# Performance work log

Measured on AMD Instinct MI355X. Metric: run time of the kernel, lower is better.

Reference implementation:

```python
import jax, jax.numpy as jnp
import numpy as np

B = 4096       # batch
D = 256        # num_features
H = 512        # proposal_hidden_units
K = 10         # mixture_components
C = 64         # context_units
L = 4          # proposal_residual_blocks
S = 10         # num_importance_samples (call default)
HEAD = 3 * K + C
LOG2PI = float(np.log(2.0 * np.pi))


def setup_inputs() -> dict:
    key = jax.random.key(0)
    ks = jax.random.split(key, 10)
    x = jax.random.normal(ks[0], (B, D), jnp.float32)
    observed_mask = (jax.random.uniform(ks[1], (B, D)) < 0.5).astype(jnp.float32)
    s_in = 1.0 / np.sqrt(2 * D)
    s_h = 1.0 / np.sqrt(H)
    W_in = (jax.random.normal(ks[2], (2 * D, H), jnp.float32) * s_in)
    b_in = jnp.zeros((H,), jnp.float32)
    W1 = jax.random.normal(ks[3], (L, H, H), jnp.float32) * s_h
    b1 = jnp.zeros((L, H), jnp.float32)
    W2 = jax.random.normal(ks[4], (L, H, H), jnp.float32) * s_h
    b2 = jnp.zeros((L, H), jnp.float32)
    W_fin = jax.random.normal(ks[5], (H, D * HEAD), jnp.float32) * s_h
    b_fin = jnp.zeros((D * HEAD,), jnp.float32)
    return {
        "x": x, "observed_mask": observed_mask,
        "W_in": W_in, "b_in": b_in,
        "W1": W1, "b1": b1, "W2": W2, "b2": b2,
        "W_fin": W_fin, "b_fin": b_fin,
        "num_importance_samples": S,
    }


def _proposal_params(x_o, observed_mask, W_in, b_in, W1, b1, W2, b2, W_fin, b_fin):
    # Residual MLP proposal network on [x_o, observed_mask].
    h = jnp.concatenate([x_o, observed_mask], axis=-1) @ W_in + b_in  # [B, H]
    for l in range(L):
        r = jax.nn.relu(h) @ W1[l] + b1[l]
        r = jax.nn.relu(r) @ W2[l] + b2[l]
        h = h + r
    out = (h @ W_fin + b_fin).reshape(h.shape[0], D, HEAD)  # [B, D, 3K+C]
    logits = out[..., :K]
    means = out[..., K:2 * K]
    scales = jax.nn.softplus(out[..., 2 * K:3 * K]) + 1e-3
    return logits, means, scales


def reference(x, observed_mask, W_in, b_in, W1, b1, W2, b2, W_fin, b_fin,
              num_importance_samples):
    query = 1.0 - observed_mask
    x_o = x * observed_mask
    x_u = x * query

    logits, means, scales = _proposal_params(
        x_o, observed_mask, W_in, b_in, W1, b1, W2, b2, W_fin, b_fin)

    # Per-feature mixture-of-Gaussians log-likelihood of x_u, masked by query.
    log_w = jax.nn.log_softmax(logits, axis=-1)               # [B, D, K]
    z = (x_u[..., None] - means) / scales
    comp_ll = -0.5 * z * z - jnp.log(scales) - 0.5 * LOG2PI   # [B, D, K]
    proposal_ll = jax.scipy.special.logsumexp(log_w + comp_ll, axis=-1) * query

    # Samples (stop_gradient in the original).
    skey = jax.random.key(1234)
    kc, kn = jax.random.split(skey)
    comp = jax.random.categorical(kc, logits, axis=-1,
                                  shape=(num_importance_samples,) + logits.shape[:2])  # [S, B, D]
    mu = jnp.take_along_axis(means[None], comp[..., None], axis=-1)[..., 0]    # [S, B, D]
    sg = jnp.take_along_axis(scales[None], comp[..., None], axis=-1)[..., 0]   # [S, B, D]
    eps = jax.random.normal(kn, comp.shape, jnp.float32)
    samples = mu + sg * eps                                   # [S, B, D]
    samples = jnp.transpose(samples, (1, 0, 2))               # [B, S, D]
    samples = jax.lax.stop_gradient(samples) * query[:, None, :]
    # call() multiplies by query twice (before and after selected_features block)
    proposal_samples = samples * query[:, None, :]

    proposal_mean = jnp.sum(jax.nn.softmax(logits, axis=-1) * means, axis=-1) * query
    proposal_mean = proposal_mean * query  # second masking, as in call()

    return proposal_ll, proposal_samples, proposal_mean
```

## Files before the change

### kernel.cpp

```cpp
#include <hip/hip_runtime.h>
#include <cstdint>

#define B 4096
#define D 256
#define H 512
#define K 10
#define NL 4
#define S 10
#define NOUT 30
#define HEADW 94
#define ND (B*D)
#define NFIN 7680
#define NLOG 2560
#define NMS  5120

typedef __bf16 bf16x8 __attribute__((ext_vector_type(8)));
typedef float  f32x16 __attribute__((ext_vector_type(16)));

__host__ __device__ inline void threefry2x32(uint32_t k0, uint32_t k1,
                                             uint32_t x0, uint32_t x1,
                                             uint32_t& o0, uint32_t& o1) {
  uint32_t ks2 = k0 ^ k1 ^ 0x1BD11BDAu;
#define TF_ROT(x, r) (((x) << (r)) | ((x) >> (32 - (r))))
#define TF_RND(r) { x0 += x1; x1 = TF_ROT(x1, r); x1 ^= x0; }
  x0 += k0; x1 += k1;
  TF_RND(13) TF_RND(15) TF_RND(26) TF_RND(6)
  x0 += k1; x1 += ks2 + 1u;
  TF_RND(17) TF_RND(29) TF_RND(16) TF_RND(24)
  x0 += ks2; x1 += k0 + 2u;
  TF_RND(13) TF_RND(15) TF_RND(26) TF_RND(6)
  x0 += k0; x1 += k1 + 3u;
  TF_RND(17) TF_RND(29) TF_RND(16) TF_RND(24)
  x0 += k1; x1 += ks2 + 4u;
  TF_RND(13) TF_RND(15) TF_RND(26) TF_RND(6)
  x0 += ks2; x1 += k0 + 5u;
  o0 = x0; o1 = x1;
#undef TF_RND
#undef TF_ROT
}

__device__ __forceinline__ uint32_t rb32(uint32_t k0, uint32_t k1, uint32_t idx) {
  uint32_t a, b;
  threefry2x32(k0, k1, 0u, idx, a, b);
  return a ^ b;
}

__device__ __forceinline__ float u01_from_bits(uint32_t bits) {
  return __uint_as_float((bits >> 9) | 0x3f800000u) - 1.0f;
}

__device__ __forceinline__ float erfinv_f32(float x) {
  float w = -log1pf(-x * x);
  float p;
  if (w < 5.0f) {
    w = w - 2.5f;
    p = 2.81022636e-08f;
    p = fmaf(p, w, 3.43273939e-07f);
    p = fmaf(p, w, -3.5233877e-06f);
    p = fmaf(p, w, -4.39150654e-06f);
    p = fmaf(p, w, 0.00021858087f);
    p = fmaf(p, w, -0.00125372503f);
    p = fmaf(p, w, -0.00417768164f);
    p = fmaf(p, w, 0.246640727f);
    p = fmaf(p, w, 1.50140941f);
  } else {
    w = sqrtf(w) - 3.0f;
    p = -0.000200214257f;
    p = fmaf(p, w, 0.000100950558f);
    p = fmaf(p, w, 0.00134934322f);
    p = fmaf(p, w, -0.00367342844f);
    p = fmaf(p, w, 0.00573950773f);
    p = fmaf(p, w, -0.0076224613f);
    p = fmaf(p, w, 0.00943887047f);
    p = fmaf(p, w, 1.00167406f);
    p = fmaf(p, w, 2.83297682f);
  }
  return p * x;
}

__device__ __forceinline__ unsigned short bf16_rne(float x) {
  uint32_t u = __float_as_uint(x);
  uint32_t r = u + 0x7fffu + ((u >> 16) & 1u);
  return (unsigned short)(r >> 16);
}

__device__ __forceinline__ void split2(float x, short& hi, short& lo) {
  unsigned short hb = bf16_rne(x);
  float hf = __uint_as_float((uint32_t)hb << 16);
  hi = (short)hb;
  lo = (short)bf16_rne(x - hf);
}

__device__ __forceinline__ void gload16(const void* g, void* l) {
  __builtin_amdgcn_global_load_lds(
      (const __attribute__((address_space(1))) void*)g,
      (__attribute__((address_space(3))) void*)l, 16, 0, 0);
}

template <int ROWS>
__device__ __forceinline__ void stage_region(const short* __restrict__ g,
                                             short* l, int wid, int lane) {
#pragma unroll
  for (int c = wid; c < ROWS / 16; c += 4) {
    const short* gp = g + (size_t)(c * 16 + (lane >> 2)) * 512 + (lane & 3) * 8;
    gload16(gp, l + c * 512);
  }
}

__global__ __launch_bounds__(256) void prep_kernel(const float* __restrict__ x,
                                                   const float* __restrict__ mask,
                                                   float* __restrict__ xcat) {
  int i = blockIdx.x * 256 + threadIdx.x;
  if (i >= B * 2 * D) return;
  int b = i >> 9, c = i & 511;
  float v = (c < D) ? x[b * D + c] * mask[b * D + c] : mask[b * D + (c - D)];
  xcat[i] = v;
}

__global__ __launch_bounds__(256) void wgatherL(const float* __restrict__ Wf,
                                                float* __restrict__ wsgL) {
  int c = blockIdx.x * 256 + threadIdx.x;
  int k = blockIdx.y;
  int dd = c / K, j = c - dd * K;
  wsgL[(size_t)k * NLOG + c] = Wf[(size_t)k * (D * HEADW) + dd * HEADW + j];
}

__global__ __launch_bounds__(256) void wsplit_ms(const float* __restrict__ Wf,
                                                 short* __restrict__ whi,
                                                 short* __restrict__ wlo) {
  __shared__ float tile[32][33];
  int n0 = blockIdx.x * 32, k0 = blockIdx.y * 32;
  int tx = threadIdx.x & 31, ty = threadIdx.x >> 5;
#pragma unroll
  for (int r = 0; r < 4; ++r) {
    int k = k0 + ty + r * 8;
    int n = n0 + tx;
    int dd = n / 20, j = n - dd * 20;
    tile[ty + r * 8][tx] = Wf[(size_t)k * (D * HEADW) + dd * HEADW + 10 + j];
  }
  __syncthreads();
#pragma unroll
  for (int r = 0; r < 4; ++r) {
    int n = n0 + ty + r * 8;
    int k = k0 + tx;
    float v = tile[tx][ty + r * 8];
    short hb, lb;
    split2(v, hb, lb);
    whi[(size_t)n * 512 + k] = hb;
    wlo[(size_t)n * 512 + k] = lb;
  }
}

template <int RELU, int RES>
__global__ __launch_bounds__(256) void gemm_trunk(const float* __restrict__ A,
                                                  const float* __restrict__ W,
                                                  const float* __restrict__ bias,
                                                  const float* res, float* C) {
  __shared__ float As[32 * 136];
  __shared__ float Ws[32 * 64];
  const int tid = threadIdx.x;
  const int lane = tid & 63, wid = tid >> 6;
  const int tx = tid & 15, ty = tid >> 4;
  const int bm = blockIdx.y * 128, bn = blockIdx.x * 64;
  const int ls = tid & 7, lm = tid >> 3;

  float acc[8][4] = {};

  for (int k0 = 0; k0 < H; k0 += 32) {
#pragma unroll
    for (int c = wid; c < 8; c += 4) {
      gload16(W + (size_t)(k0 + c * 4 + (lane >> 4)) * H + bn + (lane & 15) * 4,
              Ws + c * 256 + lane * 4);
    }
#pragma unroll
    for (int r = 0; r < 4; ++r) {
      int m = lm + 32 * r;
      float4 f = *(const float4*)(A + (size_t)(bm + m) * H + k0 + 4 * ls);
      if (RELU) {
        f.x = fmaxf(f.x, 0.0f); f.y = fmaxf(f.y, 0.0f);
        f.z = fmaxf(f.z, 0.0f); f.w = fmaxf(f.w, 0.0f);
      }
      As[(4 * ls + 0) * 136 + m] = f.x;
      As[(4 * ls + 1) * 136 + m] = f.y;
      As[(4 * ls + 2) * 136 + m] = f.z;
      As[(4 * ls + 3) * 136 + m] = f.w;
    }
    __syncthreads();
#pragma unroll
    for (int kk = 0; kk < 32; ++kk) {
      float a[8], b[4];
      *(float4*)(a + 0) = *(const float4*)(As + kk * 136 + ty * 8);
      *(float4*)(a + 4) = *(const float4*)(As + kk * 136 + ty * 8 + 4);
      *(float4*)(b + 0) = *(const float4*)(Ws + kk * 64 + tx * 4);
#pragma unroll
      for (int i = 0; i < 8; ++i)
#pragma unroll
        for (int j = 0; j < 4; ++j) acc[i][j] = fmaf(a[i], b[j], acc[i][j]);
    }
    __syncthreads();
  }
#pragma unroll
  for (int i = 0; i < 8; ++i) {
    int row = bm + ty * 8 + i;
#pragma unroll
    for (int j = 0; j < 4; ++j) {
      int col = bn + tx * 4 + j;
      float v = acc[i][j] + bias[col];
      if (RES) v = res[(size_t)row * H + col] + v;
      C[(size_t)row * H + col] = v;
    }
  }
}

__global__ __launch_bounds__(256) void gemm_logits(const float* __restrict__ A,
                                                   const float* __restrict__ Wg,
                                                   const float* __restrict__ bf,
                                                   float* __restrict__ headout) {
  __shared__ float As[32 * 136];
  __shared__ float Ws[32 * 128];
  const int tid = threadIdx.x;
  const int lane = tid & 63, wid = tid >> 6;
  const int tx = tid & 15, ty = tid >> 4;
  const int bm = blockIdx.y * 128, bn = blockIdx.x * 128;
  const int ls = tid & 7, lm = tid >> 3;

  float acc[8][8] = {};

  for (int k0 = 0; k0 < H; k0 += 32) {
#pragma unroll
    for (int c = wid; c < 16; c += 4) {
      gload16(Wg + (size_t)(k0 + c * 2 + (lane >> 5)) * NLOG + bn + (lane & 31) * 4,
              Ws + c * 256 + lane * 4);
    }
#pragma unroll
    for (int r = 0; r < 4; ++r) {
      int m = lm + 32 * r;
      float4 f = *(const float4*)(A + (size_t)(bm + m) * H + k0 + 4 * ls);
      As[(4 * ls + 0) * 136 + m] = f.x;
      As[(4 * ls + 1) * 136 + m] = f.y;
      As[(4 * ls + 2) * 136 + m] = f.z;
      As[(4 * ls + 3) * 136 + m] = f.w;
    }
    __syncthreads();
#pragma unroll
    for (int kk = 0; kk < 32; ++kk) {
      float a[8], b[8];
      *(float4*)(a + 0) = *(const float4*)(As + kk * 136 + ty * 8);
      *(float4*)(a + 4) = *(const float4*)(As + kk * 136 + ty * 8 + 4);
      *(float4*)(b + 0) = *(const float4*)(Ws + kk * 128 + tx * 8);
      *(float4*)(b + 4) = *(const float4*)(Ws + kk * 128 + tx * 8 + 4);
#pragma unroll
      for (int i = 0; i < 8; ++i)
#pragma unroll
        for (int j = 0; j < 8; ++j) acc[i][j] = fmaf(a[i], b[j], acc[i][j]);
    }
    __syncthreads();
  }
#pragma unroll
  for (int i = 0; i < 8; ++i) {
    int row = bm + ty * 8 + i;
#pragma unroll
    for (int j = 0; j < 8; ++j) {
      int c = bn + tx * 8 + j;
      int dd = c / K, jj = c - dd * K;
      float v = acc[i][j] + bf[dd * HEADW + jj];
      headout[(size_t)row * NFIN + dd * NOUT + jj] = v;
    }
  }
}

__global__ __launch_bounds__(256) void gemm_ms(const float* __restrict__ A,
                                               const short* __restrict__ Bh,
                                               const short* __restrict__ Bl,
                                               const float* __restrict__ bf,
                                               float* __restrict__ headout) {
  __shared__ short lds[4 * 128 * 32];
  const int tid = threadIdx.x;
  const int lane = tid & 63, wid = tid >> 6;
  const int wm = wid >> 1, wn = wid & 1;
  const int bm = blockIdx.y * 128, bn = blockIdx.x * 128;
  const int ls = tid & 7, lm = tid >> 3;

  short* ldsAh = lds;
  short* ldsAl = lds + 4096;
  short* ldsBh = lds + 8192;
  short* ldsBl = lds + 12288;

  const short* gBh = Bh + (size_t)bn * 512;
  const short* gBl = Bl + (size_t)bn * 512;

  f32x16 acc[2][2];
#pragma unroll
  for (int mt = 0; mt < 2; ++mt)
#pragma unroll
    for (int nt = 0; nt < 2; ++nt)
#pragma unroll
      for (int i = 0; i < 16; ++i) acc[mt][nt][i] = 0.0f;

  for (int k0 = 0; k0 < 512; k0 += 32) {
    stage_region<128>(gBh + k0, ldsBh, wid, lane);
    stage_region<128>(gBl + k0, ldsBl, wid, lane);
#pragma unroll
    for (int r = 0; r < 4; ++r) {
      int m = lm + 32 * r;
      float4 f = *(const float4*)(A + (size_t)(bm + m) * H + k0 + 4 * ls);
      short4 h4, l4;
      split2(f.x, h4.x, l4.x); split2(f.y, h4.y, l4.y);
      split2(f.z, h4.z, l4.z); split2(f.w, h4.w, l4.w);
      *(short4*)(ldsAh + m * 32 + 4 * ls) = h4;
      *(short4*)(ldsAl + m * 32 + 4 * ls) = l4;
    }
    __syncthreads();
#pragma unroll
    for (int sub = 0; sub < 2; ++sub) {
      bf16x8 ah[2], al[2], bh[2], bl[2];
#pragma unroll
      for (int mt = 0; mt < 2; ++mt) {
        int r = wm * 64 + mt * 32 + (lane & 31);
        int off = r * 32 + sub * 16 + (lane >> 5) * 8;
        ah[mt] = *(const bf16x8*)(ldsAh + off);
        al[mt] = *(const bf16x8*)(ldsAl + off);
      }
#pragma unroll
      for (int nt = 0; nt < 2; ++nt) {
        int r = wn * 64 + nt * 32 + (lane & 31);
        int off = r * 32 + sub * 16 + (lane >> 5) * 8;
        bh[nt] = *(const bf16x8*)(ldsBh + off);
        bl[nt] = *(const bf16x8*)(ldsBl + off);
      }
#pragma unroll
      for (int mt = 0; mt < 2; ++mt)
#pragma unroll
        for (int nt = 0; nt < 2; ++nt) {
          acc[mt][nt] = __builtin_amdgcn_mfma_f32_32x32x16_bf16(ah[mt], bh[nt], acc[mt][nt], 0, 0, 0);
          acc[mt][nt] = __builtin_amdgcn_mfma_f32_32x32x16_bf16(ah[mt], bl[nt], acc[mt][nt], 0, 0, 0);
          acc[mt][nt] = __builtin_amdgcn_mfma_f32_32x32x16_bf16(al[mt], bh[nt], acc[mt][nt], 0, 0, 0);
        }
    }
    __syncthreads();
  }

#pragma unroll
  for (int mt = 0; mt < 2; ++mt)
#pragma unroll
    for (int nt = 0; nt < 2; ++nt) {
      int col = bn + wn * 64 + nt * 32 + (lane & 31);
      int rbase = bm + wm * 64 + mt * 32 + 4 * (lane >> 5);
      int dd = col / 20, j = col - dd * 20;
#pragma unroll
      for (int reg = 0; reg < 16; ++reg) {
        int row = rbase + (reg & 3) + 8 * (reg >> 2);
        float v = acc[mt][nt][reg] + bf[dd * HEADW + 10 + j];
        if (j >= 10) v = (fmaxf(v, 0.0f) + log1pf(expf(-fabsf(v)))) + 0.001f;
        headout[(size_t)row * NFIN + dd * NOUT + 10 + j] = v;
      }
    }
}

__global__ __launch_bounds__(256) void fused_tail(const float* __restrict__ head,
                                                  const float* __restrict__ x,
                                                  const float* __restrict__ mask,
                                                  float* __restrict__ out_ll,
                                                  float* __restrict__ out_s,
                                                  float* __restrict__ out_mean,
                                                  uint32_t kc0, uint32_t kc1,
                                                  uint32_t kn0, uint32_t kn1) {
  int idx = blockIdx.x * 256 + threadIdx.x;
  if (idx >= ND) return;
  int b = idx >> 8, d = idx & (D - 1);
  const float* hp = head + (size_t)idx * NOUT;
  float lg[K], mn[K], sc[K];
#pragma unroll
  for (int k = 0; k < K; ++k) { lg[k] = hp[k]; mn[k] = hp[K + k]; sc[k] = hp[2 * K + k]; }
  float q = 1.0f - mask[idx];
  float xu = x[idx] * q;
  float m = lg[0];
#pragma unroll
  for (int k = 1; k < K; ++k) m = fmaxf(m, lg[k]);
  float e[K];
  float sum = 0.0f;
#pragma unroll
  for (int k = 0; k < K; ++k) { e[k] = expf(lg[k] - m); sum += e[k]; }
  float lse = logf(sum);
  float a[K];
  float amax = -3.402823466e38f;
#pragma unroll
  for (int k = 0; k < K; ++k) {
    float z = (xu - mn[k]) / sc[k];
    float cll = -0.5f * z * z - logf(sc[k]) - 0.9189385332046727f;
    float lw = (lg[k] - m) - lse;
    a[k] = lw + cll;
    amax = fmaxf(amax, a[k]);
  }
  float s2 = 0.0f;
#pragma unroll
  for (int k = 0; k < K; ++k) s2 += expf(a[k] - amax);
  out_ll[idx] = (logf(s2) + amax) * q;
  float pm = 0.0f;
#pragma unroll
  for (int k = 0; k < K; ++k) pm += (e[k] / sum) * mn[k];
  out_mean[idx] = pm * q;
  for (int s = 0; s < S; ++s) {
    uint32_t t32 = (uint32_t)s * (uint32_t)ND + (uint32_t)idx;
    uint32_t base = t32 * (uint32_t)K;
    int best = 0;
    float vbest = -3.402823466e38f;
#pragma unroll
    for (int k = 0; k < K; ++k) {
      uint32_t bits = rb32(kc0, kc1, base + (uint32_t)k);
      float f = fmaxf(u01_from_bits(bits), 1.17549435e-38f);
      float g = -logf(-logf(f));
      float v = g + lg[k];
      if (v > vbest) { vbest = v; best = k; }
    }
    uint32_t ebits = rb32(kn0, kn1, t32);
    float f = u01_from_bits(ebits);
    float r = f * 2.0f + (-0.99999994f);
    r = fmaxf(r, -0.99999994f);
    float eps = 1.4142135623730951f * erfinv_f32(r);
    out_s[((size_t)b * S + s) * D + d] = (mn[best] + sc[best] * eps) * q;
  }
}

extern "C" void kernel_launch(void* const* d_in, const int* in_sizes, int n_in,
                              void* d_out, int out_size, void* d_ws, size_t ws_size,
                              hipStream_t stream) {
  const float* x    = (const float*)d_in[0];
  const float* mask = (const float*)d_in[1];
  const float* W_in = (const float*)d_in[2];
  const float* b_in = (const float*)d_in[3];
  const float* W1   = (const float*)d_in[4];
  const float* b1   = (const float*)d_in[5];
  const float* W2   = (const float*)d_in[6];
  const float* b2   = (const float*)d_in[7];
  const float* Wf   = (const float*)d_in[8];
  const float* bf   = (const float*)d_in[9];

  char* w = (char*)d_ws;
  float* head  = (float*)w;
  float* xcat  = head;
  float* t     = head;
  float* h     = (float*)(w + 125829120);
  float* wsgL  = (float*)(w + 134217728);
  short* wms_h = (short*)(w + 139460608);
  short* wms_l = (short*)(w + 144703488);

  float* out_ll   = (float*)d_out;
  float* out_s    = out_ll + (size_t)ND;
  float* out_mean = out_s + (size_t)ND * S;

  wgatherL<<<dim3(NLOG / 256, 512), 256, 0, stream>>>(Wf, wsgL);
  wsplit_ms<<<dim3(NMS / 32, 512 / 32), 256, 0, stream>>>(Wf, wms_h, wms_l);

  prep_kernel<<<(B * 2 * D) / 256, 256, 0, stream>>>(x, mask, xcat);

  dim3 gtr(H / 64, B / 128);
  gemm_trunk<0, 0><<<gtr, 256, 0, stream>>>(xcat, W_in, b_in, nullptr, h);
  for (int l = 0; l < NL; ++l) {
    gemm_trunk<1, 0><<<gtr, 256, 0, stream>>>(h, W1 + (size_t)l * H * H,
                                              b1 + (size_t)l * H, nullptr, t);
    gemm_trunk<1, 1><<<gtr, 256, 0, stream>>>(t, W2 + (size_t)l * H * H,
                                              b2 + (size_t)l * H, h, h);
  }

  gemm_logits<<<dim3(NLOG / 128, B / 128), 256, 0, stream>>>(h, wsgL, bf, head);
  gemm_ms<<<dim3(NMS / 128, B / 128), 256, 0, stream>>>(h, wms_h, wms_l, bf, head);

  uint32_t kc0, kc1, kn0, kn1;
  threefry2x32(0u, 1234u, 0u, 0u, kc0, kc1);
  threefry2x32(0u, 1234u, 0u, 1u, kn0, kn1);
  fused_tail<<<ND / 256, 256, 0, stream>>>(head, x, mask, out_ll, out_s, out_mean,
                                           kc0, kc1, kn0, kn1);
}
```

Measured before the change: 1.322 ms.

## Load GEMM weights directly into registers and simplify Gumbel sampling

The trunk and logits GEMMs no longer stage weight tiles in shared memory. Each thread now reads its weight columns from global memory into a double-buffered register array, cutting LDS traffic and LDS allocation, at the cost of more global loads and higher register pressure. The categorical sampling replaces the Gumbel-max double log with an exponential-race argmin (-log2(u)/exp(logit)), saving one log per draw. The race is mathematically equivalent, but floating-point ties and edge cases (u=0, unnormalised e) can choose a different component than the reference.

```diff
diff --git a/kernel.cpp b/kernel.cpp
--- a/kernel.cpp
+++ b/kernel.cpp
@@ -157,21 +157,18 @@
                                                   const float* __restrict__ bias,
                                                   const float* res, float* C) {
   __shared__ float As[32 * 136];
-  __shared__ float Ws[32 * 64];
   const int tid = threadIdx.x;
-  const int lane = tid & 63, wid = tid >> 6;
   const int tx = tid & 15, ty = tid >> 4;
   const int bm = blockIdx.y * 128, bn = blockIdx.x * 64;
   const int ls = tid & 7, lm = tid >> 3;
 
+  const float* Wp = W + bn + tx * 4;
   float acc[8][4] = {};
 
   for (int k0 = 0; k0 < H; k0 += 32) {
-#pragma unroll
-    for (int c = wid; c < 8; c += 4) {
-      gload16(W + (size_t)(k0 + c * 4 + (lane >> 4)) * H + bn + (lane & 15) * 4,
-              Ws + c * 256 + lane * 4);
-    }
+    float4 bb[2][8];
+#pragma unroll
+    for (int j = 0; j < 8; ++j) bb[0][j] = *(const float4*)(Wp + (size_t)(k0 + j) * H);
 #pragma unroll
     for (int r = 0; r < 4; ++r) {
       int m = lm + 32 * r;
@@ -187,15 +184,25 @@
     }
     __syncthreads();
 #pragma unroll
-    for (int kk = 0; kk < 32; ++kk) {
-      float a[8], b[4];
-      *(float4*)(a + 0) = *(const float4*)(As + kk * 136 + ty * 8);
-      *(float4*)(a + 4) = *(const float4*)(As + kk * 136 + ty * 8 + 4);
-      *(float4*)(b + 0) = *(const float4*)(Ws + kk * 64 + tx * 4);
-#pragma unroll
-      for (int i = 0; i < 8; ++i)
-#pragma unroll
-        for (int j = 0; j < 4; ++j) acc[i][j] = fmaf(a[i], b[j], acc[i][j]);
+    for (int c = 0; c < 4; ++c) {
+      const int cb = c & 1;
+      if (c < 3) {
+#pragma unroll
+        for (int j = 0; j < 8; ++j)
+          bb[cb ^ 1][j] = *(const float4*)(Wp + (size_t)(k0 + c * 8 + 8 + j) * H);
+      }
+#pragma unroll
+      for (int j = 0; j < 8; ++j) {
+        int kk = c * 8 + j;
+        float a[8];
+        *(float4*)(a + 0) = *(const float4*)(As + kk * 136 + ty * 8);
+        *(float4*)(a + 4) = *(const float4*)(As + kk * 136 + ty * 8 + 4);
+        float b[4] = {bb[cb][j].x, bb[cb][j].y, bb[cb][j].z, bb[cb][j].w};
+#pragma unroll
+        for (int i = 0; i < 8; ++i)
+#pragma unroll
+          for (int jj = 0; jj < 4; ++jj) acc[i][jj] = fmaf(a[i], b[jj], acc[i][jj]);
+      }
     }
     __syncthreads();
   }
@@ -217,20 +224,20 @@
                                                    const float* __restrict__ bf,
                                                    float* __restrict__ headout) {
   __shared__ float As[32 * 136];
-  __shared__ float Ws[32 * 128];
   const int tid = threadIdx.x;
-  const int lane = tid & 63, wid = tid >> 6;
   const int tx = tid & 15, ty = tid >> 4;
   const int bm = blockIdx.y * 128, bn = blockIdx.x * 128;
   const int ls = tid & 7, lm = tid >> 3;
 
+  const float* Wp = Wg + bn + tx * 8;
   float acc[8][8] = {};
 
   for (int k0 = 0; k0 < H; k0 += 32) {
-#pragma unroll
-    for (int c = wid; c < 16; c += 4) {
-      gload16(Wg + (size_t)(k0 + c * 2 + (lane >> 5)) * NLOG + bn + (lane & 31) * 4,
-              Ws + c * 256 + lane * 4);
+    float4 bb[2][8];
+#pragma unroll
+    for (int j = 0; j < 4; ++j) {
+      bb[0][2 * j]     = *(const float4*)(Wp + (size_t)(k0 + j) * NLOG);
+      bb[0][2 * j + 1] = *(const float4*)(Wp + (size_t)(k0 + j) * NLOG + 4);
     }
 #pragma unroll
     for (int r = 0; r < 4; ++r) {
@@ -243,16 +250,28 @@
     }
     __syncthreads();
 #pragma unroll
-    for (int kk = 0; kk < 32; ++kk) {
-      float a[8], b[8];
-      *(float4*)(a + 0) = *(const float4*)(As + kk * 136 + ty * 8);
-      *(float4*)(a + 4) = *(const float4*)(As + kk * 136 + ty * 8 + 4);
-      *(float4*)(b + 0) = *(const float4*)(Ws + kk * 128 + tx * 8);
-      *(float4*)(b + 4) = *(const float4*)(Ws + kk * 128 + tx * 8 + 4);
-#pragma unroll
-      for (int i = 0; i < 8; ++i)
-#pragma unroll
-        for (int j = 0; j < 8; ++j) acc[i][j] = fmaf(a[i], b[j], acc[i][j]);
+    for (int c = 0; c < 8; ++c) {
+      const int cb = c & 1;
+      if (c < 7) {
+#pragma unroll
+        for (int j = 0; j < 4; ++j) {
+          bb[cb ^ 1][2 * j]     = *(const float4*)(Wp + (size_t)(k0 + c * 4 + 4 + j) * NLOG);
+          bb[cb ^ 1][2 * j + 1] = *(const float4*)(Wp + (size_t)(k0 + c * 4 + 4 + j) * NLOG + 4);
+        }
+      }
+#pragma unroll
+      for (int j = 0; j < 4; ++j) {
+        int kk = c * 4 + j;
+        float a[8], b[8];
+        *(float4*)(a + 0) = *(const float4*)(As + kk * 136 + ty * 8);
+        *(float4*)(a + 4) = *(const float4*)(As + kk * 136 + ty * 8 + 4);
+        *(float4*)(b + 0) = bb[cb][2 * j];
+        *(float4*)(b + 4) = bb[cb][2 * j + 1];
+#pragma unroll
+        for (int i = 0; i < 8; ++i)
+#pragma unroll
+          for (int jj = 0; jj < 8; ++jj) acc[i][jj] = fmaf(a[i], b[jj], acc[i][jj]);
+      }
     }
     __syncthreads();
   }
@@ -400,24 +419,27 @@
 #pragma unroll
   for (int k = 0; k < K; ++k) pm += (e[k] / sum) * mn[k];
   out_mean[idx] = pm * q;
+  float inv_e[K];
+#pragma unroll
+  for (int k = 0; k < K; ++k) inv_e[k] = 1.0f / e[k];
   for (int s = 0; s < S; ++s) {
     uint32_t t32 = (uint32_t)s * (uint32_t)ND + (uint32_t)idx;
     uint32_t base = t32 * (uint32_t)K;
     int best = 0;
-    float vbest = -3.402823466e38f;
+    float rbest = 3.402823466e38f;
 #pragma unroll
     for (int k = 0; k < K; ++k) {
       uint32_t bits = rb32(kc0, kc1, base + (uint32_t)k);
-      float f = fmaxf(u01_from_bits(bits), 1.17549435e-38f);
-      float g = -logf(-logf(f));
-      float v = g + lg[k];
-      if (v > vbest) { vbest = v; best = k; }
+      float u = u01_from_bits(bits);
+      float wv = -__log2f(u);
+      float r = wv * inv_e[k];
+      if (r < rbest) { rbest = r; best = k; }
     }
     uint32_t ebits = rb32(kn0, kn1, t32);
     float f = u01_from_bits(ebits);
-    float r = f * 2.0f + (-0.99999994f);
-    r = fmaxf(r, -0.99999994f);
-    float eps = 1.4142135623730951f * erfinv_f32(r);
+    float r2 = f * 2.0f + (-0.99999994f);
+    r2 = fmaxf(r2, -0.99999994f);
+    float eps = 1.4142135623730951f * erfinv_f32(r2);
     out_s[((size_t)b * S + s) * D + d] = (mn[best] + sc[best] * eps) * q;
   }
 }
```

After: 1.417 ms. 7.2% more time.
